# Kernel optimization log

Measured on AMD Instinct MI355X. Metric: run time of the kernel, lower is better.

## Reference

```python
import jax, jax.numpy as jnp
import numpy as np

IN_FEATURES = 1024
OUT_FEATURES = 1024
N_TOKENS = 32768


def setup_inputs() -> dict:
    key = jax.random.key(0)
    kx, kw, kb = jax.random.split(key, 3)
    x = jax.random.normal(kx, (N_TOKENS, IN_FEATURES), dtype=jnp.float32)
    weight = jax.random.normal(kw, (OUT_FEATURES, IN_FEATURES), dtype=jnp.float32)
    bias = jax.random.normal(kb, (OUT_FEATURES,), dtype=jnp.float32)
    return {"x": x, "weight": weight, "bias": bias}


def reference(x, weight, bias):
    # Binarize weights to {-1, 0, +1} via sign (matches torch.sign semantics),
    # then dense linear: y = x @ sign(W)^T + b
    bw = jnp.sign(weight)  # [out, in]
    return jnp.einsum('ni,oi->no', x, bw) + bias
```

## Files before the change

### kernel.cpp

```cpp
#include <hip/hip_runtime.h>
#include <stdint.h>

#define M_TOK 32768
#define N_OUT 1024
#define K_IN  1024

#define BM 256
#define BN 256
#define BK 64

typedef __bf16 bf16_t;
typedef bf16_t bf16x8 __attribute__((ext_vector_type(8)));
typedef float  floatx4 __attribute__((ext_vector_type(4)));

__device__ __forceinline__ unsigned short f2bf(float f) {
    uint32_t u = __float_as_uint(f);
    u += 0x7FFFu + ((u >> 16) & 1u);
    return (unsigned short)(u >> 16);
}

__global__ void cvt_x_kernel(const float* __restrict__ x, unsigned short* __restrict__ xb) {
    size_t i = (size_t)blockIdx.x * blockDim.x + threadIdx.x;
    const float4* xv = (const float4*)(x + i * 8);
    float4 a = xv[0];
    float4 b = xv[1];
    unsigned int p0 = (unsigned int)f2bf(a.x) | ((unsigned int)f2bf(a.y) << 16);
    unsigned int p1 = (unsigned int)f2bf(a.z) | ((unsigned int)f2bf(a.w) << 16);
    unsigned int p2 = (unsigned int)f2bf(b.x) | ((unsigned int)f2bf(b.y) << 16);
    unsigned int p3 = (unsigned int)f2bf(b.z) | ((unsigned int)f2bf(b.w) << 16);
    uint4 o; o.x = p0; o.y = p1; o.z = p2; o.w = p3;
    *(uint4*)(xb + i * 8) = o;
}

__global__ void cvt_w_kernel(const float* __restrict__ w, unsigned short* __restrict__ wb) {
    size_t i = (size_t)blockIdx.x * blockDim.x + threadIdx.x;
    const float4* wv = (const float4*)(w + i * 4);
    float4 a = wv[0];
    unsigned short s0 = (a.x > 0.f) ? 0x3F80u : ((a.x < 0.f) ? 0xBF80u : 0u);
    unsigned short s1 = (a.y > 0.f) ? 0x3F80u : ((a.y < 0.f) ? 0xBF80u : 0u);
    unsigned short s2 = (a.z > 0.f) ? 0x3F80u : ((a.z < 0.f) ? 0xBF80u : 0u);
    unsigned short s3 = (a.w > 0.f) ? 0x3F80u : ((a.w < 0.f) ? 0xBF80u : 0u);
    uint2 o;
    o.x = (unsigned int)s0 | ((unsigned int)s1 << 16);
    o.y = (unsigned int)s2 | ((unsigned int)s3 << 16);
    *(uint2*)(wb + i * 4) = o;
}

__device__ __forceinline__ void stage16(const unsigned short* g, unsigned short* l) {
    __builtin_amdgcn_global_load_lds(
        (const __attribute__((address_space(1))) unsigned int*)g,
        (__attribute__((address_space(3))) unsigned int*)l, 16, 0, 0);
}


#define PH_OPEN() do { asm volatile("" ::: "memory"); \
    __builtin_amdgcn_s_barrier(); \
    __builtin_amdgcn_s_setprio(1); } while(0)

#define PH_CLOSE() do { __builtin_amdgcn_s_setprio(0); \
    asm volatile("s_waitcnt lgkmcnt(0)" ::: "memory"); \
    __builtin_amdgcn_s_barrier(); } while(0)

#define PH_CLOSE_VM() do { __builtin_amdgcn_s_setprio(0); \
    asm volatile("s_waitcnt vmcnt(2)" ::: "memory"); \
    asm volatile("s_waitcnt lgkmcnt(0)" ::: "memory"); \
    __builtin_amdgcn_s_barrier(); } while(0)

#define STAGE_A(p,h,kt) do { \
    const unsigned short* _g = gAs + (size_t)((h) * 128) * K_IN + (kt) * BK; \
    unsigned short* _l = lAs + (p) * 16384 + (h) * 8192; \
    stage16(_g, _l); \
    stage16(_g + (size_t)(64 * K_IN), _l + 4096); \
} while(0)

#define STAGE_B(p,h,kt) do { \
    const unsigned short* _g = gBs + (size_t)((h) * 128) * K_IN + (kt) * BK; \
    unsigned short* _l = lBs + (p) * 16384 + (h) * 8192; \
    stage16(_g, _l); \
    stage16(_g + (size_t)(64 * K_IN), _l + 4096); \
} while(0)

#define LOAD_A(p,mh) do { _Pragma("unroll") \
    for (int mi = 0; mi < 4; ++mi) { \
        const unsigned short* _b = rA + (p) * 16384 + ((mh) * 64 + mi * 16) * 64; \
        af[mi][0] = *(const bf16x8*)(_b + gp0 * 8); \
        af[mi][1] = *(const bf16x8*)(_b + gp1 * 8); \
    } } while(0)

#define LOAD_B(p,nh) do { _Pragma("unroll") \
    for (int ni = 0; ni < 2; ++ni) { \
        const unsigned short* _b = rB + (p) * 16384 + ((nh) * 32 + ni * 16) * 64; \
        bf[(nh) * 2 + ni][0] = *(const bf16x8*)(_b + gp0 * 8); \
        bf[(nh) * 2 + ni][1] = *(const bf16x8*)(_b + gp1 * 8); \
    } } while(0)

#define MFMA_Q(mh,nh) do { _Pragma("unroll") \
    for (int mi = 0; mi < 4; ++mi) { _Pragma("unroll") \
        for (int ni = 0; ni < 2; ++ni) { \
            acc[(mh)*4+mi][(nh)*2+ni] = __builtin_amdgcn_mfma_f32_16x16x32_bf16( \
                af[mi][0], bf[(nh)*2+ni][0], acc[(mh)*4+mi][(nh)*2+ni], 0, 0, 0); \
            acc[(mh)*4+mi][(nh)*2+ni] = __builtin_amdgcn_mfma_f32_16x16x32_bf16( \
                af[mi][1], bf[(nh)*2+ni][1], acc[(mh)*4+mi][(nh)*2+ni], 0, 0, 0); \
        } } } while(0)

__global__ __launch_bounds__(512, 2) void gemm8p(
    const unsigned short* __restrict__ A,
    const unsigned short* __restrict__ B,
    const float* __restrict__ bias,
    float* __restrict__ C)
{
    extern __shared__ unsigned short lds[];
    unsigned short* sA = lds;
    unsigned short* sB = lds + 32768;

    const int t = threadIdx.x;
    const int b = blockIdx.x;
    const int wg = ((b & 7) << 6) + (b >> 3);
    const int bm = wg >> 2;
    const int bn = wg & 3;

    const int w    = t >> 6;
    const int lane = t & 63;
    const int wm   = w >> 2;
    const int wn   = w & 3;
    const int lrow = lane & 15;
    const int quad = lane >> 4;

    const int srow = (w << 3) + (lane >> 3);
    const int glog = (lane & 7) ^ (lane >> 3);
    const unsigned short* gAs = A + (size_t)(bm * BM + srow) * K_IN + glog * 8;
    const unsigned short* gBs = B + (size_t)(bn * BN + srow) * K_IN + glog * 8;
    unsigned short* lAs = sA + t * 8;
    unsigned short* lBs = sB + t * 8;

    const unsigned short* rA = sA + wm * 8192 + lrow * 64;
    const unsigned short* rB = sB + (wn >> 1) * 8192 + ((wn & 1) * 64 + lrow) * 64;
    const int gp0 = quad ^ (lrow & 7);
    const int gp1 = (4 + quad) ^ (lrow & 7);

    bf16x8  af[4][2];
    bf16x8  bf[4][2];
    floatx4 acc[8][4] = {};

    STAGE_A(0, 0, 0); STAGE_A(0, 1, 0); STAGE_B(0, 0, 0); STAGE_B(0, 1, 0);
    STAGE_A(1, 0, 1);
    asm volatile("s_waitcnt vmcnt(2)" ::: "memory");
    __builtin_amdgcn_s_barrier();

#pragma unroll 1
    for (int i = 0; i < 8; ++i) {
        const int t1 = 2 * i + 1;
        const int e  = (2 * i + 2) & 15;
        const int o  = (2 * i + 3) & 15;
        LOAD_A(0, 0); LOAD_B(0, 0); STAGE_A(1, 1, t1);
        PH_OPEN(); MFMA_Q(0, 0); PH_CLOSE();
        LOAD_B(0, 1); STAGE_B(1, 0, t1);
        PH_OPEN(); MFMA_Q(0, 1); PH_CLOSE();
        LOAD_A(0, 1); STAGE_B(1, 1, t1);
        PH_OPEN(); MFMA_Q(1, 0); PH_CLOSE();
        STAGE_A(0, 0, e);
        PH_OPEN(); MFMA_Q(1, 1); PH_CLOSE_VM();
        LOAD_A(1, 0); LOAD_B(1, 0); STAGE_A(0, 1, e);
        PH_OPEN(); MFMA_Q(0, 0); PH_CLOSE();
        LOAD_B(1, 1); STAGE_B(0, 0, e);
        PH_OPEN(); MFMA_Q(0, 1); PH_CLOSE();
        LOAD_A(1, 1); STAGE_B(0, 1, e);
        PH_OPEN(); MFMA_Q(1, 0); PH_CLOSE();
        STAGE_A(1, 0, o);
        PH_OPEN(); MFMA_Q(1, 1); PH_CLOSE_VM();
    }
    asm volatile("s_waitcnt vmcnt(0)" ::: "memory");

    const int crow0 = bm * BM + wm * 128 + quad * 4;
    const int ccol0 = bn * BN + wn * 64;
#pragma unroll
    for (int ni = 0; ni < 4; ++ni) {
        const int col = ccol0 + ni * 16 + lrow;
        const float bv = bias[col];
#pragma unroll
        for (int mi = 0; mi < 8; ++mi) {
            const int row = crow0 + mi * 16;
#pragma unroll
            for (int r = 0; r < 4; ++r)
                C[(size_t)(row + r) * N_OUT + col] = acc[mi][ni][r] + bv;
        }
    }
}

extern "C" void kernel_launch(void* const* d_in, const int* in_sizes, int n_in,
                              void* d_out, int out_size, void* d_ws, size_t ws_size,
                              hipStream_t stream) {
    const float* x    = (const float*)d_in[0];
    const float* w    = (const float*)d_in[1];
    const float* bias = (const float*)d_in[2];
    float* out        = (float*)d_out;

    unsigned short* xb = (unsigned short*)d_ws;
    unsigned short* wb = (unsigned short*)((char*)d_ws + (size_t)M_TOK * K_IN * 2);

    static bool attr_set = false;
    if (!attr_set) {
        hipFuncSetAttribute((const void*)gemm8p,
                            hipFuncAttributeMaxDynamicSharedMemorySize, 131072);
        attr_set = true;
    }

    cvt_x_kernel<<<16384, 256, 0, stream>>>(x, xb);
    cvt_w_kernel<<<1024, 256, 0, stream>>>(w, wb);
    gemm8p<<<(M_TOK / BM) * (N_OUT / BN), 512, 131072, stream>>>(xb, wb, bias, out);
}
```

Baseline: 302.7 us.

## Prefetch whole K-tiles one stage ahead and grid-stride the x conversion

The GEMM main loop no longer spreads the global-to-LDS staging of the next tile across four compute phases. It now issues a whole A+B tile load in one batch, one full tile ahead, and waits with vmcnt(8) so the other tile's loads stay in flight. This should give each tile's loads more time to land before the data is used, at the cost of burstier memory traffic. Separately, the x-to-bf16 conversion becomes a grid-stride loop launched with 2048 blocks instead of 16384, which cuts block scheduling overhead.

Result: slower. 319.4 us (+5.5%).

```diff
diff --git a/kernel.cpp b/kernel.cpp
--- a/kernel.cpp
+++ b/kernel.cpp
@@ -20,16 +20,19 @@
 }
 
 __global__ void cvt_x_kernel(const float* __restrict__ x, unsigned short* __restrict__ xb) {
-    size_t i = (size_t)blockIdx.x * blockDim.x + threadIdx.x;
-    const float4* xv = (const float4*)(x + i * 8);
-    float4 a = xv[0];
-    float4 b = xv[1];
-    unsigned int p0 = (unsigned int)f2bf(a.x) | ((unsigned int)f2bf(a.y) << 16);
-    unsigned int p1 = (unsigned int)f2bf(a.z) | ((unsigned int)f2bf(a.w) << 16);
-    unsigned int p2 = (unsigned int)f2bf(b.x) | ((unsigned int)f2bf(b.y) << 16);
-    unsigned int p3 = (unsigned int)f2bf(b.z) | ((unsigned int)f2bf(b.w) << 16);
-    uint4 o; o.x = p0; o.y = p1; o.z = p2; o.w = p3;
-    *(uint4*)(xb + i * 8) = o;
+    const size_t stride = (size_t)gridDim.x * blockDim.x;
+    const size_t ngrp = (size_t)M_TOK * K_IN / 8;
+    for (size_t i = (size_t)blockIdx.x * blockDim.x + threadIdx.x; i < ngrp; i += stride) {
+        const float4* xv = (const float4*)(x + i * 8);
+        float4 a = xv[0];
+        float4 b = xv[1];
+        unsigned int p0 = (unsigned int)f2bf(a.x) | ((unsigned int)f2bf(a.y) << 16);
+        unsigned int p1 = (unsigned int)f2bf(a.z) | ((unsigned int)f2bf(a.w) << 16);
+        unsigned int p2 = (unsigned int)f2bf(b.x) | ((unsigned int)f2bf(b.y) << 16);
+        unsigned int p3 = (unsigned int)f2bf(b.z) | ((unsigned int)f2bf(b.w) << 16);
+        uint4 o; o.x = p0; o.y = p1; o.z = p2; o.w = p3;
+        *(uint4*)(xb + i * 8) = o;
+    }
 }
 
 __global__ void cvt_w_kernel(const float* __restrict__ w, unsigned short* __restrict__ wb) {
@@ -61,8 +64,8 @@
     asm volatile("s_waitcnt lgkmcnt(0)" ::: "memory"); \
     __builtin_amdgcn_s_barrier(); } while(0)
 
-#define PH_CLOSE_VM() do { __builtin_amdgcn_s_setprio(0); \
-    asm volatile("s_waitcnt vmcnt(2)" ::: "memory"); \
+#define PH_CLOSE_VM8() do { __builtin_amdgcn_s_setprio(0); \
+    asm volatile("s_waitcnt vmcnt(8)" ::: "memory"); \
     asm volatile("s_waitcnt lgkmcnt(0)" ::: "memory"); \
     __builtin_amdgcn_s_barrier(); } while(0)
 
@@ -78,6 +81,11 @@
     unsigned short* _l = lBs + (p) * 16384 + (h) * 8192; \
     stage16(_g, _l); \
     stage16(_g + (size_t)(64 * K_IN), _l + 4096); \
+} while(0)
+
+#define STAGE_T(p,kt) do { \
+    STAGE_A(p,0,kt); STAGE_A(p,1,kt); \
+    STAGE_B(p,0,kt); STAGE_B(p,1,kt); \
 } while(0)
 
 #define LOAD_A(p,mh) do { _Pragma("unroll") \
@@ -142,32 +150,31 @@
     bf16x8  bf[4][2];
     floatx4 acc[8][4] = {};
 
-    STAGE_A(0, 0, 0); STAGE_A(0, 1, 0); STAGE_B(0, 0, 0); STAGE_B(0, 1, 0);
-    STAGE_A(1, 0, 1);
-    asm volatile("s_waitcnt vmcnt(2)" ::: "memory");
+    STAGE_T(0, 0);
+    STAGE_T(1, 1);
+    asm volatile("s_waitcnt vmcnt(8)" ::: "memory");
     __builtin_amdgcn_s_barrier();
 
 #pragma unroll 1
     for (int i = 0; i < 8; ++i) {
-        const int t1 = 2 * i + 1;
-        const int e  = (2 * i + 2) & 15;
-        const int o  = (2 * i + 3) & 15;
-        LOAD_A(0, 0); LOAD_B(0, 0); STAGE_A(1, 1, t1);
+        const int e = (2 * i + 2) & 15;
+        const int o = (2 * i + 3) & 15;
+        LOAD_A(0, 0); LOAD_B(0, 0);
         PH_OPEN(); MFMA_Q(0, 0); PH_CLOSE();
-        LOAD_B(0, 1); STAGE_B(1, 0, t1);
+        LOAD_B(0, 1);
         PH_OPEN(); MFMA_Q(0, 1); PH_CLOSE();
-        LOAD_A(0, 1); STAGE_B(1, 1, t1);
+        LOAD_A(0, 1);
         PH_OPEN(); MFMA_Q(1, 0); PH_CLOSE();
-        STAGE_A(0, 0, e);
-        PH_OPEN(); MFMA_Q(1, 1); PH_CLOSE_VM();
-        LOAD_A(1, 0); LOAD_B(1, 0); STAGE_A(0, 1, e);
+        STAGE_T(0, e);
+        PH_OPEN(); MFMA_Q(1, 1); PH_CLOSE_VM8();
+        LOAD_A(1, 0); LOAD_B(1, 0);
         PH_OPEN(); MFMA_Q(0, 0); PH_CLOSE();
-        LOAD_B(1, 1); STAGE_B(0, 0, e);
+        LOAD_B(1, 1);
         PH_OPEN(); MFMA_Q(0, 1); PH_CLOSE();
-        LOAD_A(1, 1); STAGE_B(0, 1, e);
+        LOAD_A(1, 1);
         PH_OPEN(); MFMA_Q(1, 0); PH_CLOSE();
-        STAGE_A(1, 0, o);
-        PH_OPEN(); MFMA_Q(1, 1); PH_CLOSE_VM();
+        STAGE_T(1, o);
+        PH_OPEN(); MFMA_Q(1, 1); PH_CLOSE_VM8();
     }
     asm volatile("s_waitcnt vmcnt(0)" ::: "memory");
 
@@ -205,7 +212,7 @@
         attr_set = true;
     }
 
-    cvt_x_kernel<<<16384, 256, 0, stream>>>(x, xb);
+    cvt_x_kernel<<<2048, 256, 0, stream>>>(x, xb);
     cvt_w_kernel<<<1024, 256, 0, stream>>>(w, wb);
     gemm8p<<<(M_TOK / BM) * (N_OUT / BN), 512, 131072, stream>>>(xb, wb, bias, out);
 }
```
